# Performance work log

Hardware: AMD Instinct MI355X
Metric: run time of the kernel (lower is better)

Reference implementation:

```python
import jax, jax.numpy as jnp
import numpy as np

N_POINTS = 131072
N_ANCHORS = 2048


def setup_inputs() -> dict:
    key = jax.random.key(0)
    k1, k2, k3, k4 = jax.random.split(key, 4)
    locations3d = jax.random.normal(k1, (N_POINTS, 3), dtype=jnp.float32)
    anchor_locations3d = jax.random.normal(k2, (N_ANCHORS, 3), dtype=jnp.float32)
    anchor_coeffs = jax.random.normal(k3, (N_ANCHORS,), dtype=jnp.float32)
    # per-anchor widths, kept strictly positive in [0.1, 1.0)
    anchor_parameters = jax.random.uniform(k4, (N_ANCHORS,), dtype=jnp.float32) * 0.9 + 0.1
    return {
        "locations3d": locations3d,
        "anchor_locations3d": anchor_locations3d,
        "anchor_coeffs": anchor_coeffs,
        "anchor_parameters": anchor_parameters,
    }


def potential_operator(locations3d, anchor_locations3d, anchor_parameters):
    # Pairwise squared distances via the expanded form (avoids [N,M,3] intermediate):
    x_sq = jnp.sum(locations3d * locations3d, axis=-1, keepdims=True)          # [N,1]
    a_sq = jnp.sum(anchor_locations3d * anchor_locations3d, axis=-1)            # [M]
    cross = locations3d @ anchor_locations3d.T                                  # [N,M]
    sqdist = x_sq + a_sq[None, :] - 2.0 * cross
    sqdist = jnp.maximum(sqdist, 0.0)
    inv_two_w2 = 0.5 / (anchor_parameters * anchor_parameters)                  # [M]
    return jnp.exp(-sqdist * inv_two_w2[None, :])                               # [N,M]


def reference(locations3d, anchor_locations3d, anchor_coeffs, anchor_parameters):
    K = potential_operator(locations3d, anchor_locations3d, anchor_parameters)  # [N,M]
    return K @ anchor_coeffs                                                    # [N]
```

## Files before the change

kernel.cpp:

```cpp
#include <hip/hip_runtime.h>

#define N_POINTS  131072
#define N_ANCHORS 2048
#define CHUNKS    8
#define M_PER     (N_ANCHORS / CHUNKS)
#define LOG2E     1.4426950408889634f

typedef float v2f __attribute__((ext_vector_type(2)));

__global__ __launch_bounds__(256, 8) void linear_potential_main(
    const float* __restrict__ xloc,
    const float* __restrict__ aloc,
    const float* __restrict__ coeffs,
    const float* __restrict__ params,
    float* __restrict__ out)
{
    __shared__ float4 sA[M_PER];
    __shared__ float2 sB[M_PER];

    const int t     = threadIdx.x;
    const int mbase = blockIdx.y * M_PER;

    {
        const int m  = mbase + t;
        const float a0 = aloc[3 * m + 0];
        const float a1 = aloc[3 * m + 1];
        const float a2 = aloc[3 * m + 2];
        const float w  = params[m];
        const float s  = 0.5f / (w * w);
        const float sp = -s * LOG2E;
        sA[t] = make_float4(-2.0f * sp * a0, -2.0f * sp * a1, -2.0f * sp * a2,
                            sp * (a0 * a0 + a1 * a1 + a2 * a2));
        sB[t] = make_float2(sp, coeffs[m]);
    }
    __syncthreads();

    const int tid = blockIdx.x * 256 + t;
    const int n0  = tid;
    const int n1  = tid + (N_POINTS / 2);

    const v2f xv = { xloc[3 * n0 + 0], xloc[3 * n1 + 0] };
    const v2f yv = { xloc[3 * n0 + 1], xloc[3 * n1 + 1] };
    const v2f zv = { xloc[3 * n0 + 2], xloc[3 * n1 + 2] };
    const v2f xs = xv * xv + yv * yv + zv * zv;

    v2f acc = { 0.0f, 0.0f };

    #pragma unroll 8
    for (int mm = 0; mm < M_PER; ++mm) {
        const float4 p  = sA[mm];
        const float2 tt = sB[mm];
        v2f arg = p.w + p.x * xv + p.y * yv + p.z * zv + tt.x * xs;
        arg.x = fminf(arg.x, 0.0f);
        arg.y = fminf(arg.y, 0.0f);
        v2f e = { __builtin_amdgcn_exp2f(arg.x), __builtin_amdgcn_exp2f(arg.y) };
        acc += tt.y * e;
    }

    atomicAdd(&out[n0], acc.x);
    atomicAdd(&out[n1], acc.y);
}

extern "C" void kernel_launch(void* const* d_in, const int* in_sizes, int n_in,
                              void* d_out, int out_size, void* d_ws, size_t ws_size,
                              hipStream_t stream) {
    const float* xloc   = (const float*)d_in[0];
    const float* aloc   = (const float*)d_in[1];
    const float* coeffs = (const float*)d_in[2];
    const float* params = (const float*)d_in[3];
    float* out = (float*)d_out;

    hipMemsetAsync(d_out, 0, N_POINTS * sizeof(float), stream);

    linear_potential_main<<<dim3((N_POINTS / 2) / 256, CHUNKS), dim3(256), 0, stream>>>(
        xloc, aloc, coeffs, params, out);
}
```

Before: 107.3 us.

## Compute Gaussian exponent via bf16x3-split MFMA instead of scalar FMAs

Moves the per-pair exponent computation (point-anchor cross terms plus norms) onto MFMA 16x16x32 bf16 matrix instructions. Each fp32 operand is split into three bf16 pieces to keep near-fp32 accuracy. A prep kernel packs the anchor fragments into workspace, and the main kernel reduces rows across lanes with shuffles and writes outputs directly, removing the memset and atomics. Risks: the clamp to zero on the exponent is dropped, split precision may not exactly match fp32, and the exp2 plus FMA per element still dominates.

New measurement: 92.41 us. 1.16x faster.

```diff
diff --git a/kernel.cpp b/kernel.cpp
--- a/kernel.cpp
+++ b/kernel.cpp
@@ -2,63 +2,158 @@
 
 #define N_POINTS  131072
 #define N_ANCHORS 2048
-#define CHUNKS    8
-#define M_PER     (N_ANCHORS / CHUNKS)
+#define THREADS   256
+#define PTS_BLK   128
+#define NBLOCKS   (N_POINTS / PTS_BLK)
+#define NTILES_M  (N_ANCHORS / 16)
 #define LOG2E     1.4426950408889634f
 
-typedef float v2f __attribute__((ext_vector_type(2)));
+typedef __attribute__((ext_vector_type(8))) short  short8;
+typedef __attribute__((ext_vector_type(4))) float  f32x4;
 
-__global__ __launch_bounds__(256, 8) void linear_potential_main(
+
+static __device__ __forceinline__ unsigned short f2bf(float v) {
+    union { float f; unsigned u; } c; c.f = v;
+    unsigned r = (c.u + 0x7FFFu + ((c.u >> 16) & 1u)) >> 16;
+    return (unsigned short)r;
+}
+static __device__ __forceinline__ float bf2f(unsigned short h) {
+    union { unsigned u; float f; } c; c.u = ((unsigned)h) << 16;
+    return c.f;
+}
+static __device__ __forceinline__ void split3(float v, unsigned short& h1,
+                                              unsigned short& h2, unsigned short& h3) {
+    h1 = f2bf(v); float v2 = v - bf2f(h1);
+    h2 = f2bf(v2); float v3 = v2 - bf2f(h2);
+    h3 = f2bf(v3);
+}
+
+#define BF_ONE ((short)0x3F80)
+
+__global__ void prep_B(const float* __restrict__ aloc,
+                       const float* __restrict__ coeffs,
+                       const float* __restrict__ params,
+                       short8* __restrict__ Bws,
+                       float* __restrict__ cfws) {
+    const int gid  = blockIdx.x * blockDim.x + threadIdx.x;
+    const int tile = gid >> 6;
+    const int lane = gid & 63;
+    const int kb   = lane >> 4;
+    const int m    = tile * 16 + (lane & 15);
+
+    const float a0 = aloc[3 * m + 0];
+    const float a1 = aloc[3 * m + 1];
+    const float a2 = aloc[3 * m + 2];
+    const float w  = params[m];
+    const float sp = -(0.5f * LOG2E) / (w * w);
+    const float r0 = -2.0f * sp * a0;
+    const float r1 = -2.0f * sp * a1;
+    const float r2 = -2.0f * sp * a2;
+    const float q  = sp * (a0 * a0 + a1 * a1 + a2 * a2);
+
+    unsigned short r0a, r0b, r0c, r1a, r1b, r1c, r2a, r2b, r2c, spa, spb, spc, qa, qb, qc;
+    split3(r0, r0a, r0b, r0c);
+    split3(r1, r1a, r1b, r1c);
+    split3(r2, r2a, r2b, r2c);
+    split3(sp, spa, spb, spc);
+    split3(q,  qa,  qb,  qc);
+
+    short8 fr;
+    switch (kb) {
+    case 0: fr = (short8){(short)r0a,(short)r0b,(short)r0a,(short)r0c,(short)r0a,(short)r0b,(short)r1a,(short)r1b}; break;
+    case 1: fr = (short8){(short)r1a,(short)r1c,(short)r1a,(short)r1b,(short)r2a,(short)r2b,(short)r2a,(short)r2c}; break;
+    case 2: fr = (short8){(short)r2a,(short)r2b,(short)spa,(short)spb,(short)spa,(short)spc,(short)spa,(short)spb}; break;
+    default:fr = (short8){(short)qa, (short)qb, (short)qc, 0, 0, 0, 0, 0}; break;
+    }
+    Bws[tile * 64 + lane] = fr;
+
+    if (lane < 16) cfws[m] = coeffs[m];
+}
+
+__global__ __launch_bounds__(256, 4) void lp_main(
     const float* __restrict__ xloc,
-    const float* __restrict__ aloc,
-    const float* __restrict__ coeffs,
-    const float* __restrict__ params,
+    const short8* __restrict__ Bws,
+    const float* __restrict__ cfws,
     float* __restrict__ out)
 {
-    __shared__ float4 sA[M_PER];
-    __shared__ float2 sB[M_PER];
+    __shared__ short8 sA[8][64];
 
-    const int t     = threadIdx.x;
-    const int mbase = blockIdx.y * M_PER;
+    const int t = threadIdx.x;
 
-    {
-        const int m  = mbase + t;
-        const float a0 = aloc[3 * m + 0];
-        const float a1 = aloc[3 * m + 1];
-        const float a2 = aloc[3 * m + 2];
-        const float w  = params[m];
-        const float s  = 0.5f / (w * w);
-        const float sp = -s * LOG2E;
-        sA[t] = make_float4(-2.0f * sp * a0, -2.0f * sp * a1, -2.0f * sp * a2,
-                            sp * (a0 * a0 + a1 * a1 + a2 * a2));
-        sB[t] = make_float2(sp, coeffs[m]);
+    #pragma unroll
+    for (int e0 = 0; e0 < 2; ++e0) {
+        const int e    = t + e0 * 256;
+        const int tl   = e >> 6;
+        const int lane = e & 63;
+        const int kb   = lane >> 4;
+        const int p    = blockIdx.x * PTS_BLK + tl * 16 + (lane & 15);
+
+        const float x = xloc[3 * p + 0];
+        const float y = xloc[3 * p + 1];
+        const float z = xloc[3 * p + 2];
+        const float ss = fmaf(x, x, fmaf(y, y, z * z));
+
+        unsigned short xa, xb, xc, ya, yb, yc, za, zb, zc, sa, sb, sc;
+        split3(x,  xa, xb, xc);
+        split3(y,  ya, yb, yc);
+        split3(z,  za, zb, zc);
+        split3(ss, sa, sb, sc);
+
+        short8 fr;
+        switch (kb) {
+        case 0: fr = (short8){(short)xa,(short)xa,(short)xb,(short)xa,(short)xc,(short)xb,(short)ya,(short)ya}; break;
+        case 1: fr = (short8){(short)yb,(short)ya,(short)yc,(short)yb,(short)za,(short)za,(short)zb,(short)za}; break;
+        case 2: fr = (short8){(short)zc,(short)zb,(short)sa,(short)sa,(short)sb,(short)sa,(short)sc,(short)sb}; break;
+        default:fr = (short8){BF_ONE, BF_ONE, BF_ONE, 0, 0, 0, 0, 0}; break;
+        }
+        sA[tl][lane] = fr;
     }
     __syncthreads();
 
-    const int tid = blockIdx.x * 256 + t;
-    const int n0  = tid;
-    const int n1  = tid + (N_POINTS / 2);
+    const int wave = t >> 6;
+    const int lane = t & 63;
+    const int col  = lane & 15;
 
-    const v2f xv = { xloc[3 * n0 + 0], xloc[3 * n1 + 0] };
-    const v2f yv = { xloc[3 * n0 + 1], xloc[3 * n1 + 1] };
-    const v2f zv = { xloc[3 * n0 + 2], xloc[3 * n1 + 2] };
-    const v2f xs = xv * xv + yv * yv + zv * zv;
+    const short8 a0 = sA[wave * 2 + 0][lane];
+    const short8 a1 = sA[wave * 2 + 1][lane];
 
-    v2f acc = { 0.0f, 0.0f };
+    f32x4 acc0 = {0.f, 0.f, 0.f, 0.f};
+    f32x4 acc1 = {0.f, 0.f, 0.f, 0.f};
+    const f32x4 cz = {0.f, 0.f, 0.f, 0.f};
 
-    #pragma unroll 8
-    for (int mm = 0; mm < M_PER; ++mm) {
-        const float4 p  = sA[mm];
-        const float2 tt = sB[mm];
-        v2f arg = p.w + p.x * xv + p.y * yv + p.z * zv + tt.x * xs;
-        arg.x = fminf(arg.x, 0.0f);
-        arg.y = fminf(arg.y, 0.0f);
-        v2f e = { __builtin_amdgcn_exp2f(arg.x), __builtin_amdgcn_exp2f(arg.y) };
-        acc += tt.y * e;
+    #pragma unroll 2
+    for (int tm = 0; tm < NTILES_M; ++tm) {
+        const short8 bf = Bws[tm * 64 + lane];
+        const float  cf = cfws[tm * 16 + col];
+
+        f32x4 c0 = __builtin_amdgcn_mfma_f32_16x16x32_bf16(a0, bf, cz, 0, 0, 0);
+        f32x4 c1 = __builtin_amdgcn_mfma_f32_16x16x32_bf16(a1, bf, cz, 0, 0, 0);
+
+        #pragma unroll
+        for (int r = 0; r < 4; ++r) {
+            acc0[r] = fmaf(cf, __builtin_amdgcn_exp2f(c0[r]), acc0[r]);
+            acc1[r] = fmaf(cf, __builtin_amdgcn_exp2f(c1[r]), acc1[r]);
+        }
     }
 
-    atomicAdd(&out[n0], acc.x);
-    atomicAdd(&out[n1], acc.y);
+    #pragma unroll
+    for (int o = 1; o < 16; o <<= 1) {
+        #pragma unroll
+        for (int r = 0; r < 4; ++r) {
+            acc0[r] += __shfl_xor(acc0[r], o, 16);
+            acc1[r] += __shfl_xor(acc1[r], o, 16);
+        }
+    }
+
+    if (col == 0) {
+        const int kb = lane >> 4;
+        const int pb = blockIdx.x * PTS_BLK + wave * 32;
+        #pragma unroll
+        for (int r = 0; r < 4; ++r) {
+            out[pb +      kb * 4 + r] = acc0[r];
+            out[pb + 16 + kb * 4 + r] = acc1[r];
+        }
+    }
 }
 
 extern "C" void kernel_launch(void* const* d_in, const int* in_sizes, int n_in,
@@ -70,8 +165,12 @@
     const float* params = (const float*)d_in[3];
     float* out = (float*)d_out;
 
-    hipMemsetAsync(d_out, 0, N_POINTS * sizeof(float), stream);
+    short8* Bws = (short8*)d_ws;
+    float*  cfws = (float*)((char*)d_ws + NTILES_M * 64 * sizeof(short8));
 
-    linear_potential_main<<<dim3((N_POINTS / 2) / 256, CHUNKS), dim3(256), 0, stream>>>(
-        xloc, aloc, coeffs, params, out);
+    prep_B<<<dim3((NTILES_M * 64) / THREADS), dim3(THREADS), 0, stream>>>(
+        aloc, coeffs, params, Bws, cfws);
+
+    lp_main<<<dim3(NBLOCKS), dim3(THREADS), 0, stream>>>(
+        xloc, Bws, cfws, out);
 }
```
